# Optimization experiments

Hardware: AMD Instinct MI355X
Metric: run time of the kernel (lower is better)

Reference implementation:

```python
import jax, jax.numpy as jnp
import numpy as np

T, B, I, H, L = 1024, 16, 1024, 1024, 2


def setup_inputs() -> dict:
    key = jax.random.key(0)
    ks = jax.random.split(key, 1 + 4 * L)
    k = 1.0 / np.sqrt(H)
    inp = {"x": jax.random.normal(ks[0], (T, B, I), dtype=jnp.float32)}
    for l in range(L):
        base = 1 + 4 * l
        in_dim = I if l == 0 else H
        inp[f"Wih_{l}"] = jax.random.uniform(ks[base + 0], (4 * H, in_dim), minval=-k, maxval=k, dtype=jnp.float32)
        inp[f"bih_{l}"] = jax.random.uniform(ks[base + 1], (4 * H,), minval=-k, maxval=k, dtype=jnp.float32)
        inp[f"Whh_{l}"] = jax.random.uniform(ks[base + 2], (4 * H, H), minval=-k, maxval=k, dtype=jnp.float32)
        inp[f"bhh_{l}"] = jax.random.uniform(ks[base + 3], (4 * H,), minval=-k, maxval=k, dtype=jnp.float32)
    return inp


def _lstm_layer(x, Wih, bih, Whh, bhh):
    # x: [T, B, in_dim] time-major. Returns (outputs [T,B,H], h_T [B,H], c_T [B,H]).
    Hd = Whh.shape[1]
    Bn = x.shape[1]
    h0 = jnp.zeros((Bn, Hd), dtype=x.dtype)
    c0 = jnp.zeros((Bn, Hd), dtype=x.dtype)
    # Precompute input projection for all timesteps in one big GEMM.
    gx = jnp.einsum('tbi,gi->tbg', x, Wih) + bih  # [T, B, 4H]

    def step(carry, gxt):
        h, c = carry
        gates = gxt + h @ Whh.T + bhh  # [B, 4H]
        i, f, g, o = jnp.split(gates, 4, axis=1)
        i = jax.nn.sigmoid(i)
        f = jax.nn.sigmoid(f)
        g = jnp.tanh(g)
        o = jax.nn.sigmoid(o)
        c = f * c + i * g
        h = o * jnp.tanh(c)
        return (h, c), h

    (hT, cT), ys = jax.lax.scan(step, (h0, c0), gx)
    return ys, hT, cT


def reference(x, Wih_0, bih_0, Whh_0, bhh_0, Wih_1, bih_1, Whh_1, bhh_1):
    out0, h0, c0 = _lstm_layer(x, Wih_0, bih_0, Whh_0, bhh_0)
    out1, h1, c1 = _lstm_layer(out0, Wih_1, bih_1, Whh_1, bhh_1)
    next_h = jnp.stack([h0, h1])  # [num_layers, B, H]
    next_c = jnp.stack([c0, c1])
    return out1, (next_h, next_c)
```

## Files before the change

### kernel.cpp

```cpp
#include <hip/hip_runtime.h>


#define T_STEPS 1024
#define TQ 16

typedef unsigned short u16;
typedef unsigned long long u64;
typedef __attribute__((ext_vector_type(8))) __bf16 bf16x8;
typedef __attribute__((ext_vector_type(4))) float float4v;
typedef __attribute__((ext_vector_type(4))) unsigned short ushort4v;
typedef __attribute__((ext_vector_type(8))) unsigned short ushort8;

__device__ __forceinline__ float bf2f(u16 h) {
    unsigned u = ((unsigned)h) << 16;
    return __builtin_bit_cast(float, u);
}
__device__ __forceinline__ u16 f2bf(float f) {
    unsigned u = __builtin_bit_cast(unsigned, f);
    u += 0x7fff + ((u >> 16) & 1);
    return (u16)(u >> 16);
}

__device__ __forceinline__ float4v mfma16(bf16x8 a, bf16x8 b, float4v c) {
    return __builtin_amdgcn_mfma_f32_16x16x32_bf16(a, b, c, 0, 0, 0);
}
__device__ __forceinline__ unsigned aload(const unsigned* p) {
    return __hip_atomic_load(p, __ATOMIC_RELAXED, __HIP_MEMORY_SCOPE_AGENT);
}
__device__ __forceinline__ void astore(unsigned* p, unsigned v) {
    __hip_atomic_store(p, v, __ATOMIC_RELAXED, __HIP_MEMORY_SCOPE_AGENT);
}
__device__ __forceinline__ void pin(bf16x8& v) {
    asm volatile("" : "+v"(v));
}
__device__ __forceinline__ bf16x8 gload16b(const void* p) {
    bf16x8 r;
    asm volatile("global_load_dwordx4 %0, %1, off sc0 sc1"
                 : "=v"(r) : "v"(p) : "memory");
    return r;
}
__device__ __forceinline__ void gld_lds16c(const void* g, void* l) {
    __builtin_amdgcn_global_load_lds(
        (const __attribute__((address_space(1))) unsigned*)g,
        (__attribute__((address_space(3))) unsigned*)l, 16, 0, 0);
}

__global__ void init_zero(unsigned* __restrict__ flags0,
                          unsigned* __restrict__ flags1,
                          unsigned* __restrict__ h0,
                          unsigned* __restrict__ h1) {
    int i = blockIdx.x * 256 + threadIdx.x;
    const int N0 = 65600, N1 = 256, N2 = 8192, N3 = 8192;
    for (int k = i; k < N0 + N1 + N2 + N3; k += 64 * 256) {
        if (k < N0) flags0[k] = 0u;
        else if (k < N0 + N1) flags1[k - N0] = 0u;
        else if (k < N0 + N1 + N2) h0[k - N0 - N1] = 0u;
        else h1[k - N0 - N1 - N2] = 0u;
    }
}

__device__ __forceinline__ void pack_one(const float* src, u16* dst, int tile, int rowbase) {
    int tid = threadIdx.x;
    ushort8* d = (ushort8*)dst;
#pragma unroll
    for (int it = 0; it < 8; ++it) {
        int c = tid + it * 256;
        int kc = c >> 6, lane = c & 63;
        const float4v* s4 = (const float4v*)(src + (((long)(rowbase + (lane & 15))) << 10)
                                                 + (kc << 5) + ((lane >> 4) << 3));
        float4v lo = s4[0], hi = s4[1];
        ushort8 o;
        o[0] = f2bf(lo[0]); o[1] = f2bf(lo[1]); o[2] = f2bf(lo[2]); o[3] = f2bf(lo[3]);
        o[4] = f2bf(hi[0]); o[5] = f2bf(hi[1]); o[6] = f2bf(hi[2]); o[7] = f2bf(hi[3]);
        d[tile * 2048 + c] = o;
    }
}

__global__ void pack_x(const float* __restrict__ src, u16* __restrict__ dst) {
    pack_one(src, dst, blockIdx.x, blockIdx.x << 4);
}

__global__ void pack_w(const float* __restrict__ w0, const float* __restrict__ w1,
                       const float* __restrict__ w2, const float* __restrict__ w3,
                       u16* __restrict__ d0, u16* __restrict__ d1,
                       u16* __restrict__ d2, u16* __restrict__ d3) {
    int which = blockIdx.x >> 8, tile = blockIdx.x & 255;
    const float* s = (which == 0) ? w0 : (which == 1) ? w1 : (which == 2) ? w2 : w3;
    u16* d = (which == 0) ? d0 : (which == 1) ? d1 : (which == 2) ? d2 : d3;
    int rowbase = ((tile & 3) << 10) + ((tile >> 2) << 4);
    pack_one(s, d, tile, rowbase);
}

__global__ __launch_bounds__(256, 1) void gx_gemm(
        const u16* __restrict__ xp, const bf16x8* __restrict__ wp,
        const float* __restrict__ bih, const float* __restrict__ bhh,
        u16* __restrict__ gx) {
    __shared__ u64 abuf[4096];
    __shared__ float4v part[4][4][64];
    int blk = blockIdx.x, tq = blockIdx.y;
    int tid = threadIdx.x, w = tid >> 6, L = tid & 63;
    int gc = (w << 10) + (blk << 4) + (L & 15);
    float bsum = bih[gc] + bhh[gc];

    bf16x8 wf[32];
#pragma unroll
    for (int g = 0; g < 4; ++g) {
        const bf16x8* wpt = wp + (blk * 4 + g) * 2048 + (w * 8) * 64 + L;
#pragma unroll
        for (int k = 0; k < 8; ++k) wf[g * 8 + k] = wpt[k * 64];
    }
#pragma unroll
    for (int i = 0; i < 32; ++i) pin(wf[i]);
    const bf16x8* hp = (const bf16x8*)abuf;

    const int tch = T_STEPS / TQ;
    for (int tt = 0; tt < tch; ++tt) {
        int t = tq * tch + tt;
        const char* src = (const char*)xp + ((size_t)t << 15) + (w << 13) + (L << 4);
        char* dst = (char*)abuf + (w << 13);
#pragma unroll
        for (int i = 0; i < 8; ++i) gld_lds16c(src + i * 1024, dst + i * 1024);
        __builtin_amdgcn_s_waitcnt(0);
        __builtin_amdgcn_sched_barrier(0);

        float4v acc[4];
#pragma unroll
        for (int g = 0; g < 4; ++g) acc[g] = float4v{0.f, 0.f, 0.f, 0.f};
#pragma unroll
        for (int k = 0; k < 8; ++k) {
            bf16x8 a = hp[(8 * w + k) * 64 + L];
#pragma unroll
            for (int g = 0; g < 4; ++g) acc[g] = mfma16(a, wf[g * 8 + k], acc[g]);
        }
#pragma unroll
        for (int g = 0; g < 4; ++g) part[w][g][L] = acc[g];
        __syncthreads();
        float4v s = part[0][w][L] + part[1][w][L] + part[2][w][L] + part[3][w][L];
        ushort4v o;
#pragma unroll
        for (int r = 0; r < 4; ++r) o[r] = f2bf(s[r] + bsum);
        ((ushort4v*)gx)[((t * 64 + blk) * 4 + w) * 64 + L] = o;
        __syncthreads();
    }
}

__global__ __launch_bounds__(512)
__attribute__((amdgpu_waves_per_eu(2, 2)))
void lstm_scan2(
        const u16* __restrict__ gx0,
        const bf16x8* __restrict__ wpHh0,
        const bf16x8* __restrict__ wpIh1, const bf16x8* __restrict__ wpHh1,
        const float* __restrict__ bih1, const float* __restrict__ bhh1,
        unsigned* hist0w,
        unsigned* hist1x,
        unsigned* h1s0,
        unsigned* flags0,
        unsigned* flags1,
        float* outbase) {
    __shared__ float4v lds_part[8][4][64];
    __shared__ float4v lds_g[4][64];

    int tid = threadIdx.x, w = tid >> 6, L = tid & 63;
    int m = tid >> 4, j = tid & 15;
    int Lc = ((m >> 2) << 4) | j, rr = m & 3;
    int layer = (blockIdx.x >= 64);
    int blk = blockIdx.x & 63;
    int hcol = (blk << 4) + j;
    int kcw = hcol >> 5, laneg = (hcol >> 3) & 3, jj = hcol & 7;
    int hwoff32 = ((kcw * 64 + m + (laneg << 4)) << 2) + (jj >> 1);
    float* fH = outbase + 16777216 + (layer ? 16384 : 0);
    float* fC = outbase + 16777216 + 32768 + (layer ? 16384 : 0);
    float c = 0.f;

    if (!layer) {
        bf16x8 wf[16];
#pragma unroll
        for (int g = 0; g < 4; ++g) {
            const bf16x8* wsrc = wpHh0 + (blk * 4 + g) * 2048 + (4 * w) * 64 + L;
#pragma unroll
            for (int k = 0; k < 4; ++k) wf[g * 4 + k] = wsrc[k * 64];
        }
#pragma unroll
        for (int i = 0; i < 16; ++i) pin(wf[i]);

        for (int t = 0; t < T_STEPS; ++t) {
            ushort4v gxv = {0, 0, 0, 0};
            if (w < 4) gxv = ((const ushort4v*)gx0)[((t * 64 + blk) * 4 + w) * 64 + L];
            if (t > 0) {
                unsigned v;
                do { v = aload(&flags0[t * 64 + L]); }
                while (__ballot(v != 0u) != ~0ull);
            }
            const char* base = (const char*)hist0w + ((size_t)t << 15) + (w << 12) + (L << 4);
            bf16x8 a0 = gload16b(base);
            bf16x8 a1 = gload16b(base + 1024);
            bf16x8 a2 = gload16b(base + 2048);
            bf16x8 a3 = gload16b(base + 3072);
            __builtin_amdgcn_s_waitcnt(0);
            __builtin_amdgcn_sched_barrier(0);

            float4v acc[4];
#pragma unroll
            for (int g = 0; g < 4; ++g) acc[g] = float4v{0.f, 0.f, 0.f, 0.f};
#pragma unroll
            for (int g = 0; g < 4; ++g) acc[g] = mfma16(a0, wf[g * 4 + 0], acc[g]);
#pragma unroll
            for (int g = 0; g < 4; ++g) acc[g] = mfma16(a1, wf[g * 4 + 1], acc[g]);
#pragma unroll
            for (int g = 0; g < 4; ++g) acc[g] = mfma16(a2, wf[g * 4 + 2], acc[g]);
#pragma unroll
            for (int g = 0; g < 4; ++g) acc[g] = mfma16(a3, wf[g * 4 + 3], acc[g]);
#pragma unroll
            for (int g = 0; g < 4; ++g) lds_part[w][g][L] = acc[g];
            __syncthreads();

            if (w < 4) {
                float4v s = lds_part[0][w][L] + lds_part[1][w][L]
                          + lds_part[2][w][L] + lds_part[3][w][L]
                          + lds_part[4][w][L] + lds_part[5][w][L]
                          + lds_part[6][w][L] + lds_part[7][w][L];
                float4v g4;
#pragma unroll
                for (int r = 0; r < 4; ++r) g4[r] = s[r] + bf2f(gxv[r]);
                lds_g[w][L] = g4;
            }
            __syncthreads();

            if (tid < 256) {
                float gi = lds_g[0][Lc][rr], gf = lds_g[1][Lc][rr];
                float gg = lds_g[2][Lc][rr], go = lds_g[3][Lc][rr];
                float iv = 1.f / (1.f + __expf(-gi));
                float fv = 1.f / (1.f + __expf(-gf));
                float gv = 1.f - 2.f / (1.f + __expf(2.f * gg));
                float ov = 1.f / (1.f + __expf(-go));
                c = fv * c + iv * gv;
                float h = ov * (1.f - 2.f / (1.f + __expf(2.f * c)));
                unsigned hb = f2bf(h);
                unsigned other = (unsigned)__shfl_xor((int)hb, 1);
                if (!(tid & 1))
                    astore(hist0w + ((size_t)(t + 1) << 13) + hwoff32, hb | (other << 16));
                if (t == T_STEPS - 1) {
                    fH[(m << 10) + hcol] = h;
                    fC[(m << 10) + hcol] = c;
                }
            }
            __builtin_amdgcn_s_waitcnt(0);
            __syncthreads();
            if (tid == 0) astore(&flags0[(t + 1) * 64 + blk], 1u);
        }
    } else {
        bf16x8 wf[32];
#pragma unroll
        for (int g = 0; g < 4; ++g) {
            const bf16x8* wsrc = (w < 4)
                ? (wpIh1 + (blk * 4 + g) * 2048 + (8 * w) * 64 + L)
                : (wpHh1 + (blk * 4 + g) * 2048 + (8 * (w - 4)) * 64 + L);
#pragma unroll
            for (int k = 0; k < 8; ++k) wf[g * 8 + k] = wsrc[k * 64];
        }
#pragma unroll
        for (int i = 0; i < 32; ++i) pin(wf[i]);
        int gc = (w << 10) + (blk << 4) + (L & 15);
        float bsum = (w < 4) ? (bih1[gc] + bhh1[gc]) : 0.f;

        for (int t = 0; t < T_STEPS; ++t) {
            if (w < 4) {
                unsigned v;
                do { v = aload(&flags0[(t + 1) * 64 + L]); }
                while (__ballot(v != 0u) != ~0ull);
            } else if (t > 0) {
                unsigned v;
                do { v = aload(&flags1[(t & 3) * 64 + L]); }
                while (__ballot(v == (unsigned)t) != ~0ull);
            }
            const char* base = (w < 4)
                ? ((const char*)hist0w + ((size_t)(t + 1) << 15) + (w << 13) + (L << 4))
                : ((t == 0)
                    ? ((const char*)h1s0 + ((w - 4) << 13) + (L << 4))
                    : ((const char*)hist1x + ((size_t)(t - 1) << 15) + ((w - 4) << 13) + (L << 4)));
            bf16x8 a[8];
#pragma unroll
            for (int k = 0; k < 8; ++k) a[k] = gload16b(base + k * 1024);
            __builtin_amdgcn_s_waitcnt(0);
            __builtin_amdgcn_sched_barrier(0);

            float4v acc[4];
#pragma unroll
            for (int g = 0; g < 4; ++g) acc[g] = float4v{0.f, 0.f, 0.f, 0.f};
#pragma unroll
            for (int k = 0; k < 8; ++k) {
#pragma unroll
                for (int g = 0; g < 4; ++g) acc[g] = mfma16(a[k], wf[g * 8 + k], acc[g]);
            }
#pragma unroll
            for (int g = 0; g < 4; ++g) lds_part[w][g][L] = acc[g];
            __syncthreads();

            if (w < 4) {
                float4v s = lds_part[0][w][L] + lds_part[1][w][L]
                          + lds_part[2][w][L] + lds_part[3][w][L]
                          + lds_part[4][w][L] + lds_part[5][w][L]
                          + lds_part[6][w][L] + lds_part[7][w][L];
                float4v g4;
#pragma unroll
                for (int r = 0; r < 4; ++r) g4[r] = s[r] + bsum;
                lds_g[w][L] = g4;
            }
            __syncthreads();

            float h = 0.f;
            if (tid < 256) {
                float gi = lds_g[0][Lc][rr], gf = lds_g[1][Lc][rr];
                float gg = lds_g[2][Lc][rr], go = lds_g[3][Lc][rr];
                float iv = 1.f / (1.f + __expf(-gi));
                float fv = 1.f / (1.f + __expf(-gf));
                float gv = 1.f - 2.f / (1.f + __expf(2.f * gg));
                float ov = 1.f / (1.f + __expf(-go));
                c = fv * c + iv * gv;
                h = ov * (1.f - 2.f / (1.f + __expf(2.f * c)));
                unsigned hb = f2bf(h);
                unsigned other = (unsigned)__shfl_xor((int)hb, 1);
                if (!(tid & 1))
                    astore(hist1x + ((size_t)t << 13) + hwoff32, hb | (other << 16));
            }
            __builtin_amdgcn_s_waitcnt(0);
            __syncthreads();
            if (tid == 0) astore(&flags1[(((t + 1) & 3) << 6) + blk], (unsigned)(t + 1));
            if (tid < 256) {
                outbase[(t << 14) + (m << 10) + hcol] = h;
                if (t == T_STEPS - 1) {
                    fH[(m << 10) + hcol] = h;
                    fC[(m << 10) + hcol] = c;
                }
            }
        }
    }
}

extern "C" void kernel_launch(void* const* d_in, const int* in_sizes, int n_in,
                              void* d_out, int out_size, void* d_ws, size_t ws_size,
                              hipStream_t stream) {
    const float* x    = (const float*)d_in[0];
    const float* Wih0 = (const float*)d_in[1];
    const float* bih0 = (const float*)d_in[2];
    const float* Whh0 = (const float*)d_in[3];
    const float* bhh0 = (const float*)d_in[4];
    const float* Wih1 = (const float*)d_in[5];
    const float* bih1 = (const float*)d_in[6];
    const float* Whh1 = (const float*)d_in[7];
    const float* bhh1 = (const float*)d_in[8];
    float* out = (float*)d_out;

    char* ws = (char*)d_ws;
    u16* wpIh0 = (u16*)(ws + 0);
    u16* wpHh0 = (u16*)(ws + 8388608);
    u16* wpIh1 = (u16*)(ws + 16777216);
    u16* wpHh1 = (u16*)(ws + 25165824);
    u16* xpack = (u16*)(ws + 33554432);
    u16* hist0 = (u16*)(ws + 67108864);
    u16* h1s0  = (u16*)(ws + 100696064);
    u16* gxbuf = (u16*)(ws + 100728832);
    unsigned* flags0 = (unsigned*)(ws + 234946560);
    unsigned* flags1 = (unsigned*)(ws + 235208960);

    init_zero<<<dim3(64), dim3(256), 0, stream>>>(flags0, flags1,
                                                  (unsigned*)hist0, (unsigned*)h1s0);
    pack_w<<<dim3(1024), dim3(256), 0, stream>>>(Wih0, Whh0, Wih1, Whh1,
                                                 wpIh0, wpHh0, wpIh1, wpHh1);
    pack_x<<<dim3(1024), dim3(256), 0, stream>>>(x, xpack);
    gx_gemm<<<dim3(64, TQ), dim3(256), 0, stream>>>(
        xpack, (const bf16x8*)wpIh0, bih0, bhh0, gxbuf);
    lstm_scan2<<<dim3(128), dim3(512), 0, stream>>>(
        gxbuf, (const bf16x8*)wpHh0, (const bf16x8*)wpIh1, (const bf16x8*)wpHh1,
        bih1, bhh1, (unsigned*)hist0, (unsigned*)xpack, (unsigned*)h1s0,
        flags0, flags1, out);
}
```

Before: 4.809 ms.

## Embed timestep tags in hidden-state words to replace separate flag polling

Each hidden-state pair is now stored as a 64-bit word whose upper half carries the timestep tag. Consumers poll the data itself until every tag matches, which removes the per-step waitcnt, block-wide barrier and separate flag store/load round trip. The LDS partial-sum buffer is double-buffered by timestep parity, so the trailing barrier can go. Workspace is rearranged so layer-1 history reuses the already-consumed gx buffer slot, and init_zero now clears one contiguous region. In exchange, each step moves twice the bytes for the recurrent state, correctness rests on tag uniqueness in the reused buffers, and spinning now reads the whole data vector rather than one flag.

```diff
diff --git a/kernel.cpp b/kernel.cpp
--- a/kernel.cpp
+++ b/kernel.cpp
@@ -10,6 +10,7 @@
 typedef __attribute__((ext_vector_type(4))) float float4v;
 typedef __attribute__((ext_vector_type(4))) unsigned short ushort4v;
 typedef __attribute__((ext_vector_type(8))) unsigned short ushort8;
+typedef __attribute__((ext_vector_type(4))) unsigned uint4v;
 
 __device__ __forceinline__ float bf2f(u16 h) {
     unsigned u = ((unsigned)h) << 16;
@@ -24,20 +25,14 @@
 __device__ __forceinline__ float4v mfma16(bf16x8 a, bf16x8 b, float4v c) {
     return __builtin_amdgcn_mfma_f32_16x16x32_bf16(a, b, c, 0, 0, 0);
 }
-__device__ __forceinline__ unsigned aload(const unsigned* p) {
+__device__ __forceinline__ u64 aload64(const u64* p) {
     return __hip_atomic_load(p, __ATOMIC_RELAXED, __HIP_MEMORY_SCOPE_AGENT);
 }
-__device__ __forceinline__ void astore(unsigned* p, unsigned v) {
+__device__ __forceinline__ void astore64(u64* p, u64 v) {
     __hip_atomic_store(p, v, __ATOMIC_RELAXED, __HIP_MEMORY_SCOPE_AGENT);
 }
 __device__ __forceinline__ void pin(bf16x8& v) {
     asm volatile("" : "+v"(v));
-}
-__device__ __forceinline__ bf16x8 gload16b(const void* p) {
-    bf16x8 r;
-    asm volatile("global_load_dwordx4 %0, %1, off sc0 sc1"
-                 : "=v"(r) : "v"(p) : "memory");
-    return r;
 }
 __device__ __forceinline__ void gld_lds16c(const void* g, void* l) {
     __builtin_amdgcn_global_load_lds(
@@ -45,18 +40,10 @@
         (__attribute__((address_space(3))) unsigned*)l, 16, 0, 0);
 }
 
-__global__ void init_zero(unsigned* __restrict__ flags0,
-                          unsigned* __restrict__ flags1,
-                          unsigned* __restrict__ h0,
-                          unsigned* __restrict__ h1) {
-    int i = blockIdx.x * 256 + threadIdx.x;
-    const int N0 = 65600, N1 = 256, N2 = 8192, N3 = 8192;
-    for (int k = i; k < N0 + N1 + N2 + N3; k += 64 * 256) {
-        if (k < N0) flags0[k] = 0u;
-        else if (k < N0 + N1) flags1[k - N0] = 0u;
-        else if (k < N0 + N1 + N2) h0[k - N0 - N1] = 0u;
-        else h1[k - N0 - N1 - N2] = 0u;
-    }
+__global__ void init_zero(u64* __restrict__ z) {
+    const size_t N = 4218880;
+    size_t i = (size_t)blockIdx.x * 256 + threadIdx.x;
+    for (size_t k = i; k < N; k += (size_t)256 * 256) z[k] = 0ull;
 }
 
 __device__ __forceinline__ void pack_one(const float* src, u16* dst, int tile, int rowbase) {
@@ -144,20 +131,18 @@
     }
 }
 
-__global__ __launch_bounds__(512)
-__attribute__((amdgpu_waves_per_eu(2, 2)))
+__global__ __launch_bounds__(512, 1)
 void lstm_scan2(
         const u16* __restrict__ gx0,
         const bf16x8* __restrict__ wpHh0,
         const bf16x8* __restrict__ wpIh1, const bf16x8* __restrict__ wpHh1,
         const float* __restrict__ bih1, const float* __restrict__ bhh1,
-        unsigned* hist0w,
-        unsigned* hist1x,
-        unsigned* h1s0,
-        unsigned* flags0,
-        unsigned* flags1,
+        char* hist0t,
+        char* z0,
+        char* z1,
+        char* gxb,
         float* outbase) {
-    __shared__ float4v lds_part[8][4][64];
+    __shared__ float4v lds_part[2][8][4][64];
     __shared__ float4v lds_g[4][64];
 
     int tid = threadIdx.x, w = tid >> 6, L = tid & 63;
@@ -182,43 +167,58 @@
         }
 #pragma unroll
         for (int i = 0; i < 16; ++i) pin(wf[i]);
+        int gbase = (w << 10) + (L << 2);
 
         for (int t = 0; t < T_STEPS; ++t) {
             ushort4v gxv = {0, 0, 0, 0};
             if (w < 4) gxv = ((const ushort4v*)gx0)[((t * 64 + blk) * 4 + w) * 64 + L];
+
+            const u64* sb = (t == 0) ? (const u64*)z0
+                                     : (const u64*)(hist0t + ((size_t)(t - 1) << 16));
+            u64 d[16];
             if (t > 0) {
-                unsigned v;
-                do { v = aload(&flags0[t * 64 + L]); }
-                while (__ballot(v != 0u) != ~0ull);
-            }
-            const char* base = (const char*)hist0w + ((size_t)t << 15) + (w << 12) + (L << 4);
-            bf16x8 a0 = gload16b(base);
-            bf16x8 a1 = gload16b(base + 1024);
-            bf16x8 a2 = gload16b(base + 2048);
-            bf16x8 a3 = gload16b(base + 3072);
-            __builtin_amdgcn_s_waitcnt(0);
-            __builtin_amdgcn_sched_barrier(0);
+                u64 tag = (u64)(unsigned)t;
+                u64 bad;
+                do {
+#pragma unroll
+                    for (int k = 0; k < 4; ++k)
+#pragma unroll
+                        for (int q = 0; q < 4; ++q)
+                            d[k * 4 + q] = aload64(sb + gbase + 256 * k + q);
+                    bad = 0;
+#pragma unroll
+                    for (int i = 0; i < 16; ++i) bad |= (d[i] >> 32) ^ tag;
+                } while (__ballot(bad == 0ull) != ~0ull);
+            } else {
+#pragma unroll
+                for (int k = 0; k < 4; ++k)
+#pragma unroll
+                    for (int q = 0; q < 4; ++q)
+                        d[k * 4 + q] = aload64(sb + gbase + 256 * k + q);
+            }
+            bf16x8 a[4];
+#pragma unroll
+            for (int k = 0; k < 4; ++k) {
+                uint4v v = { (unsigned)d[4 * k], (unsigned)d[4 * k + 1],
+                             (unsigned)d[4 * k + 2], (unsigned)d[4 * k + 3] };
+                a[k] = __builtin_bit_cast(bf16x8, v);
+            }
 
             float4v acc[4];
 #pragma unroll
             for (int g = 0; g < 4; ++g) acc[g] = float4v{0.f, 0.f, 0.f, 0.f};
 #pragma unroll
-            for (int g = 0; g < 4; ++g) acc[g] = mfma16(a0, wf[g * 4 + 0], acc[g]);
-#pragma unroll
-            for (int g = 0; g < 4; ++g) acc[g] = mfma16(a1, wf[g * 4 + 1], acc[g]);
-#pragma unroll
-            for (int g = 0; g < 4; ++g) acc[g] = mfma16(a2, wf[g * 4 + 2], acc[g]);
-#pragma unroll
-            for (int g = 0; g < 4; ++g) acc[g] = mfma16(a3, wf[g * 4 + 3], acc[g]);
-#pragma unroll
-            for (int g = 0; g < 4; ++g) lds_part[w][g][L] = acc[g];
+            for (int k = 0; k < 4; ++k)
+#pragma unroll
+                for (int g = 0; g < 4; ++g) acc[g] = mfma16(a[k], wf[g * 4 + k], acc[g]);
+#pragma unroll
+            for (int g = 0; g < 4; ++g) lds_part[t & 1][w][g][L] = acc[g];
             __syncthreads();
 
             if (w < 4) {
-                float4v s = lds_part[0][w][L] + lds_part[1][w][L]
-                          + lds_part[2][w][L] + lds_part[3][w][L]
-                          + lds_part[4][w][L] + lds_part[5][w][L]
-                          + lds_part[6][w][L] + lds_part[7][w][L];
+                float4v s = lds_part[t & 1][0][w][L];
+#pragma unroll
+                for (int ks = 1; ks < 8; ++ks) s = s + lds_part[t & 1][ks][w][L];
                 float4v g4;
 #pragma unroll
                 for (int r = 0; r < 4; ++r) g4[r] = s[r] + bf2f(gxv[r]);
@@ -238,15 +238,13 @@
                 unsigned hb = f2bf(h);
                 unsigned other = (unsigned)__shfl_xor((int)hb, 1);
                 if (!(tid & 1))
-                    astore(hist0w + ((size_t)(t + 1) << 13) + hwoff32, hb | (other << 16));
+                    astore64((u64*)(hist0t + ((size_t)t << 16) + ((size_t)hwoff32 << 3)),
+                             (u64)(hb | (other << 16)) | ((u64)(unsigned)(t + 1) << 32));
                 if (t == T_STEPS - 1) {
                     fH[(m << 10) + hcol] = h;
                     fC[(m << 10) + hcol] = c;
                 }
             }
-            __builtin_amdgcn_s_waitcnt(0);
-            __syncthreads();
-            if (tid == 0) astore(&flags0[(t + 1) * 64 + blk], 1u);
         }
     } else {
         bf16x8 wf[32];
@@ -262,45 +260,60 @@
         for (int i = 0; i < 32; ++i) pin(wf[i]);
         int gc = (w << 10) + (blk << 4) + (L & 15);
         float bsum = (w < 4) ? (bih1[gc] + bhh1[gc]) : 0.f;
+        int gbase = ((w & 3) << 11) + (L << 2);
 
         for (int t = 0; t < T_STEPS; ++t) {
+            const u64* sb;
+            u64 tag;
+            if (w < 4) { sb = (const u64*)(hist0t + ((size_t)t << 16)); tag = (u64)(unsigned)(t + 1); }
+            else {
+                sb = (t == 0) ? (const u64*)z1
+                              : (const u64*)(gxb + ((size_t)(t - 1) << 17));
+                tag = (u64)(unsigned)t;
+            }
+            u64 d[32];
+            if (w < 4 || t > 0) {
+                u64 bad;
+                do {
+#pragma unroll
+                    for (int k = 0; k < 8; ++k)
+#pragma unroll
+                        for (int q = 0; q < 4; ++q)
+                            d[k * 4 + q] = aload64(sb + gbase + 256 * k + q);
+                    bad = 0;
+#pragma unroll
+                    for (int i = 0; i < 32; ++i) bad |= (d[i] >> 32) ^ tag;
+                } while (__ballot(bad == 0ull) != ~0ull);
+            } else {
+#pragma unroll
+                for (int k = 0; k < 8; ++k)
+#pragma unroll
+                    for (int q = 0; q < 4; ++q)
+                        d[k * 4 + q] = aload64(sb + gbase + 256 * k + q);
+            }
+            bf16x8 a[8];
+#pragma unroll
+            for (int k = 0; k < 8; ++k) {
+                uint4v v = { (unsigned)d[4 * k], (unsigned)d[4 * k + 1],
+                             (unsigned)d[4 * k + 2], (unsigned)d[4 * k + 3] };
+                a[k] = __builtin_bit_cast(bf16x8, v);
+            }
+
+            float4v acc[4];
+#pragma unroll
+            for (int g = 0; g < 4; ++g) acc[g] = float4v{0.f, 0.f, 0.f, 0.f};
+#pragma unroll
+            for (int k = 0; k < 8; ++k)
+#pragma unroll
+                for (int g = 0; g < 4; ++g) acc[g] = mfma16(a[k], wf[g * 8 + k], acc[g]);
+#pragma unroll
+            for (int g = 0; g < 4; ++g) lds_part[t & 1][w][g][L] = acc[g];
+            __syncthreads();
+
             if (w < 4) {
-                unsigned v;
-                do { v = aload(&flags0[(t + 1) * 64 + L]); }
-                while (__ballot(v != 0u) != ~0ull);
-            } else if (t > 0) {
-                unsigned v;
-                do { v = aload(&flags1[(t & 3) * 64 + L]); }
-                while (__ballot(v == (unsigned)t) != ~0ull);
-            }
-            const char* base = (w < 4)
-                ? ((const char*)hist0w + ((size_t)(t + 1) << 15) + (w << 13) + (L << 4))
-                : ((t == 0)
-                    ? ((const char*)h1s0 + ((w - 4) << 13) + (L << 4))
-                    : ((const char*)hist1x + ((size_t)(t - 1) << 15) + ((w - 4) << 13) + (L << 4)));
-            bf16x8 a[8];
-#pragma unroll
-            for (int k = 0; k < 8; ++k) a[k] = gload16b(base + k * 1024);
-            __builtin_amdgcn_s_waitcnt(0);
-            __builtin_amdgcn_sched_barrier(0);
-
-            float4v acc[4];
-#pragma unroll
-            for (int g = 0; g < 4; ++g) acc[g] = float4v{0.f, 0.f, 0.f, 0.f};
-#pragma unroll
-            for (int k = 0; k < 8; ++k) {
-#pragma unroll
-                for (int g = 0; g < 4; ++g) acc[g] = mfma16(a[k], wf[g * 8 + k], acc[g]);
-            }
-#pragma unroll
-            for (int g = 0; g < 4; ++g) lds_part[w][g][L] = acc[g];
-            __syncthreads();
-
-            if (w < 4) {
-                float4v s = lds_part[0][w][L] + lds_part[1][w][L]
-                          + lds_part[2][w][L] + lds_part[3][w][L]
-                          + lds_part[4][w][L] + lds_part[5][w][L]
-                          + lds_part[6][w][L] + lds_part[7][w][L];
+                float4v s = lds_part[t & 1][0][w][L];
+#pragma unroll
+                for (int ks = 1; ks < 8; ++ks) s = s + lds_part[t & 1][ks][w][L];
                 float4v g4;
 #pragma unroll
                 for (int r = 0; r < 4; ++r) g4[r] = s[r] + bsum;
@@ -321,12 +334,8 @@
                 unsigned hb = f2bf(h);
                 unsigned other = (unsigned)__shfl_xor((int)hb, 1);
                 if (!(tid & 1))
-                    astore(hist1x + ((size_t)t << 13) + hwoff32, hb | (other << 16));
-            }
-            __builtin_amdgcn_s_waitcnt(0);
-            __syncthreads();
-            if (tid == 0) astore(&flags1[(((t + 1) & 3) << 6) + blk], (unsigned)(t + 1));
-            if (tid < 256) {
+                    astore64((u64*)(gxb + ((size_t)t << 17) + ((size_t)hwoff32 << 3)),
+                             (u64)(hb | (other << 16)) | ((u64)(unsigned)(t + 1) << 32));
                 outbase[(t << 14) + (m << 10) + hcol] = h;
                 if (t == T_STEPS - 1) {
                     fH[(m << 10) + hcol] = h;
@@ -356,22 +365,20 @@
     u16* wpHh0 = (u16*)(ws + 8388608);
     u16* wpIh1 = (u16*)(ws + 16777216);
     u16* wpHh1 = (u16*)(ws + 25165824);
+    char* hist0t = ws + 33554432;
     u16* xpack = (u16*)(ws + 33554432);
-    u16* hist0 = (u16*)(ws + 67108864);
-    u16* h1s0  = (u16*)(ws + 100696064);
-    u16* gxbuf = (u16*)(ws + 100728832);
-    unsigned* flags0 = (unsigned*)(ws + 234946560);
-    unsigned* flags1 = (unsigned*)(ws + 235208960);
-
-    init_zero<<<dim3(64), dim3(256), 0, stream>>>(flags0, flags1,
-                                                  (unsigned*)hist0, (unsigned*)h1s0);
+    u64* tailz = (u64*)(ws + 67108864);
+    char* z0   = ws + 100728832;
+    char* z1   = ws + 100794368;
+    char* gxb  = ws + 100859904;
+
+    init_zero<<<dim3(256), dim3(256), 0, stream>>>(tailz);
     pack_w<<<dim3(1024), dim3(256), 0, stream>>>(Wih0, Whh0, Wih1, Whh1,
                                                  wpIh0, wpHh0, wpIh1, wpHh1);
     pack_x<<<dim3(1024), dim3(256), 0, stream>>>(x, xpack);
     gx_gemm<<<dim3(64, TQ), dim3(256), 0, stream>>>(
-        xpack, (const bf16x8*)wpIh0, bih0, bhh0, gxbuf);
+        xpack, (const bf16x8*)wpIh0, bih0, bhh0, (u16*)gxb);
     lstm_scan2<<<dim3(128), dim3(512), 0, stream>>>(
-        gxbuf, (const bf16x8*)wpHh0, (const bf16x8*)wpIh1, (const bf16x8*)wpHh1,
-        bih1, bhh1, (unsigned*)hist0, (unsigned*)xpack, (unsigned*)h1s0,
-        flags0, flags1, out);
-}
+        (const u16*)gxb, (const bf16x8*)wpHh0, (const bf16x8*)wpIh1,
+        (const bf16x8*)wpHh1, bih1, bhh1, hist0t, z0, z1, gxb, out);
+}
```

Result: slower. 9.482 ms (+97.2%).
